# Performance work log

Measured on AMD Instinct MI355X. Metric: run time of the kernel, lower is better.

Reference implementation:

```python
import jax, jax.numpy as jnp
import numpy as np

N_NODES = 50000
N_EDGES = 1600000
IN_DIM, HID_DIM, OUT_DIM = 512, 128, 16


def spmm(edge_src, edge_dst, edge_vals, x):
    # sparse.mm(A, x): out[dst] += A[dst, src] * x[src]
    msgs = edge_vals[:, None] * x[edge_src]  # [E, D]
    return jax.ops.segment_sum(msgs, edge_dst, num_segments=N_NODES)


def setup_inputs() -> dict:
    key = jax.random.key(0)
    k1, k2, k3, k4, k5, k6 = jax.random.split(key, 6)
    feature = jax.random.normal(k1, (N_NODES, IN_DIM), dtype=jnp.float32)
    edge_src = jax.random.randint(k2, (N_EDGES,), 0, N_NODES, dtype=jnp.int32)
    edge_dst = jax.random.randint(k3, (N_EDGES,), 0, N_NODES, dtype=jnp.int32)
    edge_vals = jax.random.uniform(k4, (N_EDGES,), dtype=jnp.float32)
    # kaiming_uniform-style init: bound = sqrt(6 / fan_in) (a=sqrt(5) omitted for simplicity of scale)
    b1 = float(np.sqrt(6.0 / IN_DIM))
    b2 = float(np.sqrt(6.0 / HID_DIM))
    W1 = jax.random.uniform(k5, (IN_DIM, HID_DIM), dtype=jnp.float32, minval=-b1, maxval=b1)
    W2 = jax.random.uniform(k6, (HID_DIM, OUT_DIM), dtype=jnp.float32, minval=-b2, maxval=b2)
    return {"feature": feature, "edge_src": edge_src, "edge_dst": edge_dst,
            "edge_vals": edge_vals, "W1": W1, "W2": W2}


def reference(feature, edge_src, edge_dst, edge_vals, W1, W2):
    # layer 1: dense matmul -> sparse aggregation -> ReLU
    h = jax.nn.relu(spmm(edge_src, edge_dst, edge_vals, feature @ W1))
    # layer 2
    out = spmm(edge_src, edge_dst, edge_vals, h @ W2)
    return out
```

## Files before the change

### kernel.cpp

```cpp
#include <hip/hip_runtime.h>

#define N_NODES 50000
#define N_EDGES 1600000
#define IN_DIM 512
#define HID_DIM 128
#define OUT_DIM 16

#define BKT_SHIFT 6
#define BKT_NODES 64
#define NB ((N_NODES + BKT_NODES - 1) / BKT_NODES)
#define SC_BLOCKS ((N_EDGES + 4095) / 4096)
#define PREP_BLOCKS ((IN_DIM * HID_DIM + 1023) / 1024)
#define NS_CAP 2560

typedef __attribute__((ext_vector_type(8))) __bf16 bf16x8;
typedef __attribute__((ext_vector_type(4))) __bf16 bf16x4;
typedef __attribute__((ext_vector_type(8))) unsigned short ushort8;
typedef __attribute__((ext_vector_type(4))) float f32x4;
typedef __attribute__((ext_vector_type(2))) float f32x2;

static __device__ __forceinline__ unsigned short f2bf(float x) {
    unsigned int u = __float_as_uint(x);
    u += 0x7FFFu + ((u >> 16) & 1u);
    return (unsigned short)(u >> 16);
}
static __device__ __forceinline__ float bf2f(unsigned short v) {
    return __uint_as_float(((unsigned int)v) << 16);
}
static __device__ __forceinline__ unsigned char f2fp8(float x) {
    int pk = __builtin_amdgcn_cvt_pk_fp8_f32(x, x, 0, false);
    return (unsigned char)(pk & 0xFF);
}

__device__ inline int wave_incl_scan(int v) {
    #pragma unroll
    for (int off = 1; off < 64; off <<= 1) {
        int x = __shfl_up(v, off, 64);
        if ((threadIdx.x & 63) >= off) v += x;
    }
    return v;
}


__global__ void zero_bcnt_kernel(int* __restrict__ bcnt) {
    int t = threadIdx.x;
    if (t < NB) bcnt[t] = 0;
}

__global__ __launch_bounds__(1024) void hist_prep_kernel(const int* __restrict__ dst,
                                                         int* __restrict__ bcnt,
                                                         int* __restrict__ blk_hist_T,
                                                         const float* __restrict__ W1,
                                                         unsigned short* __restrict__ Wt) {
    if (blockIdx.x >= SC_BLOCKS) {
        int i = (blockIdx.x - SC_BLOCKS) * 1024 + threadIdx.x;
        if (i < IN_DIM * HID_DIM) {
            int k = i >> 7, col = i & 127;
            Wt[(size_t)col * IN_DIM + k] = f2bf(W1[i]);
        }
        return;
    }
    __shared__ int lc[NB];
    const int t = threadIdx.x;
    for (int b = t; b < NB; b += 1024) lc[b] = 0;
    __syncthreads();
    const int eb = blockIdx.x * 4096 + t * 4;
    if (eb + 4 <= N_EDGES) {
        int4 d4 = *(const int4*)&dst[eb];
        atomicAdd(&lc[d4.x >> BKT_SHIFT], 1);
        atomicAdd(&lc[d4.y >> BKT_SHIFT], 1);
        atomicAdd(&lc[d4.z >> BKT_SHIFT], 1);
        atomicAdd(&lc[d4.w >> BKT_SHIFT], 1);
    } else {
        for (int k = 0; k < 4; k++) {
            int e = eb + k;
            if (e < N_EDGES) atomicAdd(&lc[dst[e] >> BKT_SHIFT], 1);
        }
    }
    __syncthreads();
    for (int b = t; b < NB; b += 1024) {
        int c = lc[b];
        blk_hist_T[(size_t)b * SC_BLOCKS + blockIdx.x] = c;
        if (c) atomicAdd(&bcnt[b], c);
    }
}

__global__ __launch_bounds__(1024) void bucket_scan_kernel(const int* __restrict__ bcnt,
                                                           int* __restrict__ bucket_ptr) {
    __shared__ int wsums[16];
    const int t = threadIdx.x;
    const int lane = t & 63, wid = t >> 6;
    int v = (t < NB) ? bcnt[t] : 0;
    int incl = wave_incl_scan(v);
    if (lane == 63) wsums[wid] = incl;
    __syncthreads();
    if (wid == 0) {
        int wv = (lane < 16) ? wsums[lane] : 0;
        int ws = wave_incl_scan(wv);
        if (lane < 16) wsums[lane] = ws;
    }
    __syncthreads();
    int woff = wid ? wsums[wid - 1] : 0;
    int excl = woff + incl - v;
    if (t < NB) bucket_ptr[t] = excl;
    if (t == NB - 1) bucket_ptr[NB] = excl + v;
}

__global__ __launch_bounds__(512) void base_scan_kernel(const int* __restrict__ bucket_ptr,
                                                        int* __restrict__ blk_hist_T) {
    const int lane = threadIdx.x & 63;
    const int b = blockIdx.x * 8 + (threadIdx.x >> 6);
    if (b >= NB) return;
    int* row = blk_hist_T + (size_t)b * SC_BLOCKS;
    int carry = bucket_ptr[b];
    for (int c0 = 0; c0 < SC_BLOCKS; c0 += 64) {
        int idx = c0 + lane;
        int v = (idx < SC_BLOCKS) ? row[idx] : 0;
        int incl = wave_incl_scan(v);
        if (idx < SC_BLOCKS) row[idx] = carry + incl - v;
        carry += __shfl(incl, 63, 64);
    }
}

__global__ __launch_bounds__(1024) void bucket_scatter_kernel(const int* __restrict__ src,
                                                              const int* __restrict__ dst,
                                                              const float* __restrict__ val,
                                                              const int* __restrict__ blk_hist_T,
                                                              int2* __restrict__ pairs_bkt) {
    __shared__ int cbase[NB];
    const int t = threadIdx.x;
    for (int b = t; b < NB; b += 1024)
        cbase[b] = blk_hist_T[(size_t)b * SC_BLOCKS + blockIdx.x];
    __syncthreads();
    const int eb = blockIdx.x * 4096 + t * 4;
    if (eb + 4 <= N_EDGES) {
        int4 s4 = *(const int4*)&src[eb];
        int4 d4 = *(const int4*)&dst[eb];
        float4 v4 = *(const float4*)&val[eb];
        #pragma unroll
        for (int k = 0; k < 4; k++) {
            int ss = (k == 0) ? s4.x : (k == 1) ? s4.y : (k == 2) ? s4.z : s4.w;
            int dd = (k == 0) ? d4.x : (k == 1) ? d4.y : (k == 2) ? d4.z : d4.w;
            float vv = (k == 0) ? v4.x : (k == 1) ? v4.y : (k == 2) ? v4.z : v4.w;
            int b = dd >> BKT_SHIFT, dl = dd & (BKT_NODES - 1);
            int pos = atomicAdd(&cbase[b], 1);
            int2 pr;
            pr.x = ss | (dl << 16);
            pr.y = __float_as_int(vv);
            pairs_bkt[pos] = pr;
        }
    } else {
        for (int k = 0; k < 4; k++) {
            int e = eb + k;
            if (e < N_EDGES) {
                int dd = dst[e];
                int b = dd >> BKT_SHIFT, dl = dd & (BKT_NODES - 1);
                int pos = atomicAdd(&cbase[b], 1);
                int2 pr;
                pr.x = src[e] | (dl << 16);
                pr.y = __float_as_int(val[e]);
                pairs_bkt[pos] = pr;
            }
        }
    }
}

__global__ __launch_bounds__(512) void node_sort_fused_kernel(const int2* __restrict__ pairs_bkt,
                                                              const int* __restrict__ bucket_ptr,
                                                              int* __restrict__ row_ptr,
                                                              int2* __restrict__ pairs) {
    __shared__ int cnt[BKT_NODES];
    __shared__ int base[BKT_NODES];
    __shared__ int2 stage[NS_CAP];
    const int t = threadIdx.x;
    const int b = blockIdx.x;
    const int s = bucket_ptr[b], e = bucket_ptr[b + 1];
    if (t < BKT_NODES) cnt[t] = 0;
    __syncthreads();
    for (int i = s + t; i < e; i += 512)
        atomicAdd(&cnt[pairs_bkt[i].x >> 16], 1);
    __syncthreads();
    if (t < BKT_NODES) {
        int v = cnt[t];
        int incl = wave_incl_scan(v);
        base[t] = s + incl - v;
    }
    __syncthreads();
    if (t < BKT_NODES) {
        int n = b * BKT_NODES + t;
        if (n < N_NODES) row_ptr[n] = base[t];
        cnt[t] = 0;
    }
    if (b == NB - 1 && t == 0) row_ptr[N_NODES] = N_EDGES;
    __syncthreads();
    for (int i = s + t; i < e; i += 512) {
        int2 pr = pairs_bkt[i];
        int dl = pr.x >> 16;
        int p = base[dl] + atomicAdd(&cnt[dl], 1);
        int loc = p - s;
        if (loc < NS_CAP) stage[loc] = pr;
        else pairs[p] = pr;
    }
    __syncthreads();
    const int lim = min(e - s, NS_CAP);
    for (int j = t; j < lim; j += 512)
        pairs[s + j] = stage[j];
}


#define G1_XSTR 72
#define G1_BSTR 72
__global__ __launch_bounds__(512) void gemm1_kernel(const float* __restrict__ X,
                                                    const unsigned short* __restrict__ Wt,
                                                    unsigned char* __restrict__ h0) {
    __shared__ __align__(16) unsigned short Xs[128 * G1_XSTR];
    __shared__ __align__(16) unsigned short Bs[128 * G1_BSTR];
    const int t = threadIdx.x;
    const int lane = t & 63;
    const int wave = t >> 6;
    const int wr = wave >> 2;
    const int wc = wave & 3;
    const int c = lane & 15, g = lane >> 4;
    const int m0 = blockIdx.x * 128;

    f32x4 acc[4][2];
    #pragma unroll
    for (int mt = 0; mt < 4; mt++)
        #pragma unroll
        for (int nt = 0; nt < 2; nt++) acc[mt][nt] = (f32x4){0.f, 0.f, 0.f, 0.f};

    float4 xr[4];
    ushort8 br[2];

    #define G1_LOAD(kt)                                                                  \
        _Pragma("unroll")                                                                \
        for (int p = 0; p < 4; p++) {                                                    \
            int idx = p * 512 + t;                                                       \
            int xrow = idx >> 4, xseg = idx & 15;                                        \
            int grow = m0 + xrow; grow = (grow < N_NODES) ? grow : (N_NODES - 1);        \
            xr[p] = *(const float4*)&X[(size_t)grow * IN_DIM + (kt) * 64 + xseg * 4];    \
        }                                                                                \
        _Pragma("unroll")                                                                \
        for (int p = 0; p < 2; p++) {                                                    \
            int idx = p * 512 + t;                                                       \
            int bcol = idx >> 3, bseg = idx & 7;                                         \
            br[p] = *(const ushort8*)&Wt[(size_t)bcol * IN_DIM + (kt) * 64 + bseg * 8];  \
        }

    G1_LOAD(0)
    for (int kt = 0; kt < 8; kt++) {
        #pragma unroll
        for (int p = 0; p < 4; p++) {
            int idx = p * 512 + t;
            int xrow = idx >> 4, xseg = idx & 15;
            bf16x4 xw;
            xw[0] = (__bf16)xr[p].x; xw[1] = (__bf16)xr[p].y;
            xw[2] = (__bf16)xr[p].z; xw[3] = (__bf16)xr[p].w;
            *(bf16x4*)&Xs[xrow * G1_XSTR + xseg * 4] = xw;
        }
        #pragma unroll
        for (int p = 0; p < 2; p++) {
            int idx = p * 512 + t;
            int bcol = idx >> 3, bseg = idx & 7;
            *(ushort8*)&Bs[bcol * G1_BSTR + bseg * 8] = br[p];
        }
        __syncthreads();
        if (kt < 7) G1_LOAD(kt + 1)
        #pragma unroll
        for (int ks = 0; ks < 2; ks++) {
            bf16x8 bf[2];
            #pragma unroll
            for (int nt = 0; nt < 2; nt++) {
                int col = wc * 32 + nt * 16 + c;
                bf[nt] = *(const bf16x8*)&Bs[col * G1_BSTR + ks * 32 + g * 8];
            }
            #pragma unroll
            for (int mt = 0; mt < 4; mt++) {
                bf16x8 af = *(const bf16x8*)&Xs[(wr * 64 + mt * 16 + c) * G1_XSTR + ks * 32 + g * 8];
                #pragma unroll
                for (int nt = 0; nt < 2; nt++)
                    acc[mt][nt] = __builtin_amdgcn_mfma_f32_16x16x32_bf16(af, bf[nt],
                                                                          acc[mt][nt], 0, 0, 0);
            }
        }
        __syncthreads();
    }
    #undef G1_LOAD

    #pragma unroll
    for (int mt = 0; mt < 4; mt++) {
        #pragma unroll
        for (int r = 0; r < 4; r++) {
            int row = m0 + wr * 64 + mt * 16 + g * 4 + r;
            if (row < N_NODES) {
                #pragma unroll
                for (int nt = 0; nt < 2; nt++) {
                    int col = wc * 32 + nt * 16 + c;
                    h0[(size_t)row * HID_DIM + col] = f2fp8(acc[mt][nt][r]);
                }
            }
        }
    }
}

__global__ __launch_bounds__(256) void spmm1_node_kernel(const unsigned char* __restrict__ h0,
                                                         const int* __restrict__ row_ptr,
                                                         const int2* __restrict__ pairs,
                                                         unsigned short* __restrict__ h) {
    const int wid = __builtin_amdgcn_readfirstlane(threadIdx.x >> 6);
    const int n = blockIdx.x * 4 + wid;
    const int lane = threadIdx.x & 63;
    const int s = row_ptr[n], e = row_ptr[n + 1];
    const unsigned char* h0l = h0 + lane * 2;
    float ax = 0.f, ay = 0.f;
    for (int base = s; base < e; base += 8) {
        float vv[8];
        const unsigned char* rp[8];
        #pragma unroll
        for (int k = 0; k < 8; k++) {
            int idx = base + k;
            int cidx = (idx < e) ? idx : (e - 1);
            int2 pr = pairs[cidx];
            vv[k] = (idx < e) ? __int_as_float(pr.y) : 0.f;
            rp[k] = h0l + (size_t)(pr.x & 0xFFFF) * HID_DIM;
        }
        unsigned short gg[8];
        #pragma unroll
        for (int k = 0; k < 8; k++) gg[k] = *(const unsigned short*)rp[k];
        #pragma unroll
        for (int k = 0; k < 8; k++) {
            f32x2 f = __builtin_amdgcn_cvt_pk_f32_fp8((int)gg[k], false);
            ax += vv[k] * f.x;
            ay += vv[k] * f.y;
        }
    }
    unsigned int w = ((unsigned int)f2bf(fmaxf(ay, 0.f)) << 16) | f2bf(fmaxf(ax, 0.f));
    ((unsigned int*)(h + (size_t)n * HID_DIM))[lane] = w;
}

__global__ __launch_bounds__(256) void gemm2_kernel(const unsigned short* __restrict__ H,
                                                    const float* __restrict__ W2,
                                                    unsigned short* __restrict__ C) {
    __shared__ float Hs[16][132];
    __shared__ float Ws[128][16];
    const int t = threadIdx.x;
    const int n0 = blockIdx.x * 16;
    #pragma unroll
    for (int p = 0; p < 2; p++) {
        int idx = p * 256 + t;
        ((float4*)Ws)[idx] = ((const float4*)W2)[idx];
    }
    {
        int row = t >> 4, seg = t & 15;
        int gr = n0 + row;
        ushort8 hv = {0, 0, 0, 0, 0, 0, 0, 0};
        if (gr < N_NODES) hv = *(const ushort8*)&H[(size_t)gr * HID_DIM + seg * 8];
        #pragma unroll
        for (int j = 0; j < 8; j++) Hs[row][seg * 8 + j] = bf2f(hv[j]);
    }
    __syncthreads();
    const int nl = t >> 4, j = t & 15;
    float acc = 0.f;
    #pragma unroll 8
    for (int k = 0; k < 128; k++) acc += Hs[nl][k] * Ws[k][j];
    int n = n0 + nl;
    if (n < N_NODES) C[(size_t)n * OUT_DIM + j] = f2bf(acc);
}

__global__ __launch_bounds__(256) void spmm2_node_kernel(const unsigned short* __restrict__ h2,
                                                         const int* __restrict__ row_ptr,
                                                         const int2* __restrict__ pairs,
                                                         float* __restrict__ out) {
    const int idx = blockIdx.x * 256 + threadIdx.x;
    const int n = idx >> 4;
    const int d = idx & 15;
    if (n >= N_NODES) return;
    const int s = row_ptr[n], e = row_ptr[n + 1];
    float acc = 0.f;
    int i = s;
    for (; i + 4 <= e; i += 4) {
        int2 p0 = pairs[i], p1 = pairs[i + 1], p2 = pairs[i + 2], p3 = pairs[i + 3];
        unsigned short g0 = h2[(size_t)(p0.x & 0xFFFF) * OUT_DIM + d];
        unsigned short g1 = h2[(size_t)(p1.x & 0xFFFF) * OUT_DIM + d];
        unsigned short g2 = h2[(size_t)(p2.x & 0xFFFF) * OUT_DIM + d];
        unsigned short g3 = h2[(size_t)(p3.x & 0xFFFF) * OUT_DIM + d];
        acc += __int_as_float(p0.y) * bf2f(g0) + __int_as_float(p1.y) * bf2f(g1)
             + __int_as_float(p2.y) * bf2f(g2) + __int_as_float(p3.y) * bf2f(g3);
    }
    for (; i < e; i++) {
        int2 pr = pairs[i];
        acc += __int_as_float(pr.y) * bf2f(h2[(size_t)(pr.x & 0xFFFF) * OUT_DIM + d]);
    }
    out[(size_t)n * OUT_DIM + d] = acc;
}


extern "C" void kernel_launch(void* const* d_in, const int* in_sizes, int n_in,
                              void* d_out, int out_size, void* d_ws, size_t ws_size,
                              hipStream_t stream) {
    const float* feature   = (const float*)d_in[0];
    const int*   edge_src  = (const int*)d_in[1];
    const int*   edge_dst  = (const int*)d_in[2];
    const float* edge_vals = (const float*)d_in[3];
    const float* W1        = (const float*)d_in[4];
    const float* W2        = (const float*)d_in[5];
    float* out = (float*)d_out;

    char* ws = (char*)d_ws;
    size_t off = 0;
    auto alloc = [&](size_t bytes) {
        void* p = ws + off;
        off += (bytes + 255) & ~(size_t)255;
        return p;
    };
    unsigned char*  h0    = (unsigned char*)alloc((size_t)N_NODES * HID_DIM);
    unsigned short* Wt    = (unsigned short*)alloc((size_t)IN_DIM * HID_DIM * 2);
    unsigned short* h     = (unsigned short*)alloc((size_t)N_NODES * HID_DIM * 2);
    unsigned short* h2    = (unsigned short*)alloc((size_t)N_NODES * OUT_DIM * 2);
    int*   bcnt           = (int*)alloc((size_t)NB * 4);
    int*   bucket_ptr     = (int*)alloc((size_t)(NB + 1) * 4);
    int*   blk_hist_T     = (int*)alloc((size_t)NB * SC_BLOCKS * 4);
    int*   row_ptr        = (int*)alloc((size_t)(N_NODES + 1) * 4);
    int2*  pairs_bkt      = (int2*)alloc((size_t)N_EDGES * 8);
    int2*  pairs          = (int2*)alloc((size_t)N_EDGES * 8);

    zero_bcnt_kernel<<<1, 1024, 0, stream>>>(bcnt);
    hist_prep_kernel<<<SC_BLOCKS + PREP_BLOCKS, 1024, 0, stream>>>(edge_dst, bcnt, blk_hist_T,
                                                                   W1, Wt);
    bucket_scan_kernel<<<1, 1024, 0, stream>>>(bcnt, bucket_ptr);
    base_scan_kernel<<<(NB + 7) / 8, 512, 0, stream>>>(bucket_ptr, blk_hist_T);
    bucket_scatter_kernel<<<SC_BLOCKS, 1024, 0, stream>>>(edge_src, edge_dst, edge_vals,
                                                          blk_hist_T, pairs_bkt);
    node_sort_fused_kernel<<<NB, 512, 0, stream>>>(pairs_bkt, bucket_ptr, row_ptr, pairs);

    gemm1_kernel<<<(N_NODES + 127) / 128, 512, 0, stream>>>(feature, Wt, h0);
    spmm1_node_kernel<<<(N_NODES + 3) / 4, 256, 0, stream>>>(h0, row_ptr, pairs, h);
    gemm2_kernel<<<(N_NODES + 15) / 16, 256, 0, stream>>>(h, W2, h2);
    spmm2_node_kernel<<<(N_NODES * 16 + 255) / 256, 256, 0, stream>>>(h2, row_ptr, pairs, out);
}
```

Measured before the change: 146.5 us.

## Merge bucket scatter with gemm1 launch and fuse gemm2 into spmm1 epilogue

Measured after the change: 168.6 us. 15.1% more time.

```diff
diff --git a/kernel.cpp b/kernel.cpp
--- a/kernel.cpp
+++ b/kernel.cpp
@@ -12,6 +12,7 @@
 #define SC_BLOCKS ((N_EDGES + 4095) / 4096)
 #define PREP_BLOCKS ((IN_DIM * HID_DIM + 1023) / 1024)
 #define NS_CAP 2560
+#define MG_GEMM_BLOCKS ((N_NODES + 127) / 128)
 
 typedef __attribute__((ext_vector_type(8))) __bf16 bf16x8;
 typedef __attribute__((ext_vector_type(4))) __bf16 bf16x4;
@@ -122,44 +123,146 @@
     }
 }
 
-__global__ __launch_bounds__(1024) void bucket_scatter_kernel(const int* __restrict__ src,
-                                                              const int* __restrict__ dst,
-                                                              const float* __restrict__ val,
-                                                              const int* __restrict__ blk_hist_T,
-                                                              int2* __restrict__ pairs_bkt) {
-    __shared__ int cbase[NB];
-    const int t = threadIdx.x;
-    for (int b = t; b < NB; b += 1024)
-        cbase[b] = blk_hist_T[(size_t)b * SC_BLOCKS + blockIdx.x];
-    __syncthreads();
-    const int eb = blockIdx.x * 4096 + t * 4;
-    if (eb + 4 <= N_EDGES) {
-        int4 s4 = *(const int4*)&src[eb];
-        int4 d4 = *(const int4*)&dst[eb];
-        float4 v4 = *(const float4*)&val[eb];
-        #pragma unroll
-        for (int k = 0; k < 4; k++) {
-            int ss = (k == 0) ? s4.x : (k == 1) ? s4.y : (k == 2) ? s4.z : s4.w;
-            int dd = (k == 0) ? d4.x : (k == 1) ? d4.y : (k == 2) ? d4.z : d4.w;
-            float vv = (k == 0) ? v4.x : (k == 1) ? v4.y : (k == 2) ? v4.z : v4.w;
-            int b = dd >> BKT_SHIFT, dl = dd & (BKT_NODES - 1);
-            int pos = atomicAdd(&cbase[b], 1);
-            int2 pr;
-            pr.x = ss | (dl << 16);
-            pr.y = __float_as_int(vv);
-            pairs_bkt[pos] = pr;
+
+#define G1_XSTR 72
+#define G1_BSTR 72
+__global__ __launch_bounds__(512) void scatter_gemm1_kernel(const float* __restrict__ X,
+                                                            const unsigned short* __restrict__ Wt,
+                                                            unsigned char* __restrict__ h0,
+                                                            const int* __restrict__ src,
+                                                            const int* __restrict__ dst,
+                                                            const float* __restrict__ val,
+                                                            const int* __restrict__ blk_hist_T,
+                                                            int2* __restrict__ pairs_bkt) {
+    if (blockIdx.x < MG_GEMM_BLOCKS) {
+        __shared__ __align__(16) unsigned short Xs[128 * G1_XSTR];
+        __shared__ __align__(16) unsigned short Bs[128 * G1_BSTR];
+        const int t = threadIdx.x;
+        const int lane = t & 63;
+        const int wave = t >> 6;
+        const int wr = wave >> 2;
+        const int wc = wave & 3;
+        const int c = lane & 15, g = lane >> 4;
+        const int m0 = blockIdx.x * 128;
+
+        f32x4 acc[4][2];
+        #pragma unroll
+        for (int mt = 0; mt < 4; mt++)
+            #pragma unroll
+            for (int nt = 0; nt < 2; nt++) acc[mt][nt] = (f32x4){0.f, 0.f, 0.f, 0.f};
+
+        float4 xr[4];
+        ushort8 br[2];
+
+        #define G1_LOAD(kt)                                                                  \
+            _Pragma("unroll")                                                                \
+            for (int p = 0; p < 4; p++) {                                                    \
+                int idx = p * 512 + t;                                                       \
+                int xrow = idx >> 4, xseg = idx & 15;                                        \
+                int grow = m0 + xrow; grow = (grow < N_NODES) ? grow : (N_NODES - 1);        \
+                xr[p] = *(const float4*)&X[(size_t)grow * IN_DIM + (kt) * 64 + xseg * 4];    \
+            }                                                                                \
+            _Pragma("unroll")                                                                \
+            for (int p = 0; p < 2; p++) {                                                    \
+                int idx = p * 512 + t;                                                       \
+                int bcol = idx >> 3, bseg = idx & 7;                                         \
+                br[p] = *(const ushort8*)&Wt[(size_t)bcol * IN_DIM + (kt) * 64 + bseg * 8];  \
+            }
+
+        G1_LOAD(0)
+        for (int kt = 0; kt < 8; kt++) {
+            #pragma unroll
+            for (int p = 0; p < 4; p++) {
+                int idx = p * 512 + t;
+                int xrow = idx >> 4, xseg = idx & 15;
+                bf16x4 xw;
+                xw[0] = (__bf16)xr[p].x; xw[1] = (__bf16)xr[p].y;
+                xw[2] = (__bf16)xr[p].z; xw[3] = (__bf16)xr[p].w;
+                *(bf16x4*)&Xs[xrow * G1_XSTR + xseg * 4] = xw;
+            }
+            #pragma unroll
+            for (int p = 0; p < 2; p++) {
+                int idx = p * 512 + t;
+                int bcol = idx >> 3, bseg = idx & 7;
+                *(ushort8*)&Bs[bcol * G1_BSTR + bseg * 8] = br[p];
+            }
+            __syncthreads();
+            if (kt < 7) G1_LOAD(kt + 1)
+            #pragma unroll
+            for (int ks = 0; ks < 2; ks++) {
+                bf16x8 bf[2];
+                #pragma unroll
+                for (int nt = 0; nt < 2; nt++) {
+                    int col = wc * 32 + nt * 16 + c;
+                    bf[nt] = *(const bf16x8*)&Bs[col * G1_BSTR + ks * 32 + g * 8];
+                }
+                #pragma unroll
+                for (int mt = 0; mt < 4; mt++) {
+                    bf16x8 af = *(const bf16x8*)&Xs[(wr * 64 + mt * 16 + c) * G1_XSTR + ks * 32 + g * 8];
+                    #pragma unroll
+                    for (int nt = 0; nt < 2; nt++)
+                        acc[mt][nt] = __builtin_amdgcn_mfma_f32_16x16x32_bf16(af, bf[nt],
+                                                                              acc[mt][nt], 0, 0, 0);
+                }
+            }
+            __syncthreads();
+        }
+        #undef G1_LOAD
+
+        #pragma unroll
+        for (int mt = 0; mt < 4; mt++) {
+            #pragma unroll
+            for (int r = 0; r < 4; r++) {
+                int row = m0 + wr * 64 + mt * 16 + g * 4 + r;
+                if (row < N_NODES) {
+                    #pragma unroll
+                    for (int nt = 0; nt < 2; nt++) {
+                        int col = wc * 32 + nt * 16 + c;
+                        h0[(size_t)row * HID_DIM + col] = f2fp8(acc[mt][nt][r]);
+                    }
+                }
+            }
         }
     } else {
-        for (int k = 0; k < 4; k++) {
-            int e = eb + k;
-            if (e < N_EDGES) {
-                int dd = dst[e];
-                int b = dd >> BKT_SHIFT, dl = dd & (BKT_NODES - 1);
-                int pos = atomicAdd(&cbase[b], 1);
-                int2 pr;
-                pr.x = src[e] | (dl << 16);
-                pr.y = __float_as_int(val[e]);
-                pairs_bkt[pos] = pr;
+        __shared__ int cbase[NB];
+        const int sb = blockIdx.x - MG_GEMM_BLOCKS;
+        const int t = threadIdx.x;
+        for (int b = t; b < NB; b += 512)
+            cbase[b] = blk_hist_T[(size_t)b * SC_BLOCKS + sb];
+        __syncthreads();
+        const int eb = sb * 4096 + t * 8;
+        #pragma unroll
+        for (int half = 0; half < 2; half++) {
+            int e0 = eb + half * 4;
+            if (e0 + 4 <= N_EDGES) {
+                int4 s4 = *(const int4*)&src[e0];
+                int4 d4 = *(const int4*)&dst[e0];
+                float4 v4 = *(const float4*)&val[e0];
+                #pragma unroll
+                for (int k = 0; k < 4; k++) {
+                    int ss = (k == 0) ? s4.x : (k == 1) ? s4.y : (k == 2) ? s4.z : s4.w;
+                    int dd = (k == 0) ? d4.x : (k == 1) ? d4.y : (k == 2) ? d4.z : d4.w;
+                    float vv = (k == 0) ? v4.x : (k == 1) ? v4.y : (k == 2) ? v4.z : v4.w;
+                    int b = dd >> BKT_SHIFT, dl = dd & (BKT_NODES - 1);
+                    int pos = atomicAdd(&cbase[b], 1);
+                    int2 pr;
+                    pr.x = ss | (dl << 16);
+                    pr.y = __float_as_int(vv);
+                    pairs_bkt[pos] = pr;
+                }
+            } else {
+                for (int k = 0; k < 4; k++) {
+                    int e = e0 + k;
+                    if (e < N_EDGES) {
+                        int dd = dst[e];
+                        int b = dd >> BKT_SHIFT, dl = dd & (BKT_NODES - 1);
+                        int pos = atomicAdd(&cbase[b], 1);
+                        int2 pr;
+                        pr.x = src[e] | (dl << 16);
+                        pr.y = __float_as_int(val[e]);
+                        pairs_bkt[pos] = pr;
+                    }
+                }
             }
         }
     }
@@ -207,106 +310,20 @@
         pairs[s + j] = stage[j];
 }
 
-
-#define G1_XSTR 72
-#define G1_BSTR 72
-__global__ __launch_bounds__(512) void gemm1_kernel(const float* __restrict__ X,
-                                                    const unsigned short* __restrict__ Wt,
-                                                    unsigned char* __restrict__ h0) {
-    __shared__ __align__(16) unsigned short Xs[128 * G1_XSTR];
-    __shared__ __align__(16) unsigned short Bs[128 * G1_BSTR];
+__global__ __launch_bounds__(256) void spmm1_fused_kernel(const unsigned char* __restrict__ h0,
+                                                          const int* __restrict__ row_ptr,
+                                                          const int2* __restrict__ pairs,
+                                                          const float* __restrict__ W2,
+                                                          unsigned short* __restrict__ h2) {
+    __shared__ float W2s[HID_DIM][OUT_DIM + 1];
     const int t = threadIdx.x;
-    const int lane = t & 63;
-    const int wave = t >> 6;
-    const int wr = wave >> 2;
-    const int wc = wave & 3;
-    const int c = lane & 15, g = lane >> 4;
-    const int m0 = blockIdx.x * 128;
-
-    f32x4 acc[4][2];
     #pragma unroll
-    for (int mt = 0; mt < 4; mt++)
-        #pragma unroll
-        for (int nt = 0; nt < 2; nt++) acc[mt][nt] = (f32x4){0.f, 0.f, 0.f, 0.f};
-
-    float4 xr[4];
-    ushort8 br[2];
-
-    #define G1_LOAD(kt)                                                                  \
-        _Pragma("unroll")                                                                \
-        for (int p = 0; p < 4; p++) {                                                    \
-            int idx = p * 512 + t;                                                       \
-            int xrow = idx >> 4, xseg = idx & 15;                                        \
-            int grow = m0 + xrow; grow = (grow < N_NODES) ? grow : (N_NODES - 1);        \
-            xr[p] = *(const float4*)&X[(size_t)grow * IN_DIM + (kt) * 64 + xseg * 4];    \
-        }                                                                                \
-        _Pragma("unroll")                                                                \
-        for (int p = 0; p < 2; p++) {                                                    \
-            int idx = p * 512 + t;                                                       \
-            int bcol = idx >> 3, bseg = idx & 7;                                         \
-            br[p] = *(const ushort8*)&Wt[(size_t)bcol * IN_DIM + (kt) * 64 + bseg * 8];  \
-        }
-
-    G1_LOAD(0)
-    for (int kt = 0; kt < 8; kt++) {
-        #pragma unroll
-        for (int p = 0; p < 4; p++) {
-            int idx = p * 512 + t;
-            int xrow = idx >> 4, xseg = idx & 15;
-            bf16x4 xw;
-            xw[0] = (__bf16)xr[p].x; xw[1] = (__bf16)xr[p].y;
-            xw[2] = (__bf16)xr[p].z; xw[3] = (__bf16)xr[p].w;
-            *(bf16x4*)&Xs[xrow * G1_XSTR + xseg * 4] = xw;
-        }
-        #pragma unroll
-        for (int p = 0; p < 2; p++) {
-            int idx = p * 512 + t;
-            int bcol = idx >> 3, bseg = idx & 7;
-            *(ushort8*)&Bs[bcol * G1_BSTR + bseg * 8] = br[p];
-        }
-        __syncthreads();
-        if (kt < 7) G1_LOAD(kt + 1)
-        #pragma unroll
-        for (int ks = 0; ks < 2; ks++) {
-            bf16x8 bf[2];
-            #pragma unroll
-            for (int nt = 0; nt < 2; nt++) {
-                int col = wc * 32 + nt * 16 + c;
-                bf[nt] = *(const bf16x8*)&Bs[col * G1_BSTR + ks * 32 + g * 8];
-            }
-            #pragma unroll
-            for (int mt = 0; mt < 4; mt++) {
-                bf16x8 af = *(const bf16x8*)&Xs[(wr * 64 + mt * 16 + c) * G1_XSTR + ks * 32 + g * 8];
-                #pragma unroll
-                for (int nt = 0; nt < 2; nt++)
-                    acc[mt][nt] = __builtin_amdgcn_mfma_f32_16x16x32_bf16(af, bf[nt],
-                                                                          acc[mt][nt], 0, 0, 0);
-            }
-        }
-        __syncthreads();
-    }
-    #undef G1_LOAD
-
-    #pragma unroll
-    for (int mt = 0; mt < 4; mt++) {
-        #pragma unroll
-        for (int r = 0; r < 4; r++) {
-            int row = m0 + wr * 64 + mt * 16 + g * 4 + r;
-            if (row < N_NODES) {
-                #pragma unroll
-                for (int nt = 0; nt < 2; nt++) {
-                    int col = wc * 32 + nt * 16 + c;
-                    h0[(size_t)row * HID_DIM + col] = f2fp8(acc[mt][nt][r]);
-                }
-            }
-        }
-    }
-}
-
-__global__ __launch_bounds__(256) void spmm1_node_kernel(const unsigned char* __restrict__ h0,
-                                                         const int* __restrict__ row_ptr,
-                                                         const int2* __restrict__ pairs,
-                                                         unsigned short* __restrict__ h) {
+    for (int p = 0; p < 8; p++) {
+        int idx = p * 256 + t;
+        W2s[idx >> 4][idx & 15] = W2[idx];
+    }
+    __syncthreads();
+
     const int wid = __builtin_amdgcn_readfirstlane(threadIdx.x >> 6);
     const int n = blockIdx.x * 4 + wid;
     const int lane = threadIdx.x & 63;
@@ -334,37 +351,26 @@
             ay += vv[k] * f.y;
         }
     }
-    unsigned int w = ((unsigned int)f2bf(fmaxf(ay, 0.f)) << 16) | f2bf(fmaxf(ax, 0.f));
-    ((unsigned int*)(h + (size_t)n * HID_DIM))[lane] = w;
-}
-
-__global__ __launch_bounds__(256) void gemm2_kernel(const unsigned short* __restrict__ H,
-                                                    const float* __restrict__ W2,
-                                                    unsigned short* __restrict__ C) {
-    __shared__ float Hs[16][132];
-    __shared__ float Ws[128][16];
-    const int t = threadIdx.x;
-    const int n0 = blockIdx.x * 16;
+    const float hx = fmaxf(ax, 0.f), hy = fmaxf(ay, 0.f);
+
+    float p[OUT_DIM];
     #pragma unroll
-    for (int p = 0; p < 2; p++) {
-        int idx = p * 256 + t;
-        ((float4*)Ws)[idx] = ((const float4*)W2)[idx];
-    }
-    {
-        int row = t >> 4, seg = t & 15;
-        int gr = n0 + row;
-        ushort8 hv = {0, 0, 0, 0, 0, 0, 0, 0};
-        if (gr < N_NODES) hv = *(const ushort8*)&H[(size_t)gr * HID_DIM + seg * 8];
-        #pragma unroll
-        for (int j = 0; j < 8; j++) Hs[row][seg * 8 + j] = bf2f(hv[j]);
-    }
-    __syncthreads();
-    const int nl = t >> 4, j = t & 15;
-    float acc = 0.f;
-    #pragma unroll 8
-    for (int k = 0; k < 128; k++) acc += Hs[nl][k] * Ws[k][j];
-    int n = n0 + nl;
-    if (n < N_NODES) C[(size_t)n * OUT_DIM + j] = f2bf(acc);
+    for (int j = 0; j < OUT_DIM; j++)
+        p[j] = hx * W2s[2 * lane][j] + hy * W2s[2 * lane + 1][j];
+    #pragma unroll
+    for (int m = 1; m < 64; m <<= 1)
+        #pragma unroll
+        for (int j = 0; j < OUT_DIM; j++)
+            p[j] += __shfl_xor(p[j], m, 64);
+
+    if (lane == 0) {
+        ushort8 o0, o1;
+        #pragma unroll
+        for (int j = 0; j < 8; j++) { o0[j] = f2bf(p[j]); o1[j] = f2bf(p[8 + j]); }
+        ushort8* dstp = (ushort8*)&h2[(size_t)n * OUT_DIM];
+        dstp[0] = o0;
+        dstp[1] = o1;
+    }
 }
 
 __global__ __launch_bounds__(256) void spmm2_node_kernel(const unsigned short* __restrict__ h2,
@@ -415,7 +421,6 @@
     };
     unsigned char*  h0    = (unsigned char*)alloc((size_t)N_NODES * HID_DIM);
     unsigned short* Wt    = (unsigned short*)alloc((size_t)IN_DIM * HID_DIM * 2);
-    unsigned short* h     = (unsigned short*)alloc((size_t)N_NODES * HID_DIM * 2);
     unsigned short* h2    = (unsigned short*)alloc((size_t)N_NODES * OUT_DIM * 2);
     int*   bcnt           = (int*)alloc((size_t)NB * 4);
     int*   bucket_ptr     = (int*)alloc((size_t)(NB + 1) * 4);
@@ -429,12 +434,10 @@
                                                                    W1, Wt);
     bucket_scan_kernel<<<1, 1024, 0, stream>>>(bcnt, bucket_ptr);
     base_scan_kernel<<<(NB + 7) / 8, 512, 0, stream>>>(bucket_ptr, blk_hist_T);
-    bucket_scatter_kernel<<<SC_BLOCKS, 1024, 0, stream>>>(edge_src, edge_dst, edge_vals,
-                                                          blk_hist_T, pairs_bkt);
+    scatter_gemm1_kernel<<<MG_GEMM_BLOCKS + SC_BLOCKS, 512, 0, stream>>>(
+        feature, Wt, h0, edge_src, edge_dst, edge_vals, blk_hist_T, pairs_bkt);
     node_sort_fused_kernel<<<NB, 512, 0, stream>>>(pairs_bkt, bucket_ptr, row_ptr, pairs);
 
-    gemm1_kernel<<<(N_NODES + 127) / 128, 512, 0, stream>>>(feature, Wt, h0);
-    spmm1_node_kernel<<<(N_NODES + 3) / 4, 256, 0, stream>>>(h0, row_ptr, pairs, h);
-    gemm2_kernel<<<(N_NODES + 15) / 16, 256, 0, stream>>>(h, W2, h2);
+    spmm1_fused_kernel<<<(N_NODES + 3) / 4, 256, 0, stream>>>(h0, row_ptr, pairs, W2, h2);
     spmm2_node_kernel<<<(N_NODES * 16 + 255) / 256, 256, 0, stream>>>(h2, row_ptr, pairs, out);
 }
```

## Merge bucket scatter into gemm1 launch as heterogeneous blocks

Applied to the files above, without the earlier changes.

After: 143.9 us. No clear change (-1.8%).

```diff
diff --git a/kernel.cpp b/kernel.cpp
--- a/kernel.cpp
+++ b/kernel.cpp
@@ -12,6 +12,7 @@
 #define SC_BLOCKS ((N_EDGES + 4095) / 4096)
 #define PREP_BLOCKS ((IN_DIM * HID_DIM + 1023) / 1024)
 #define NS_CAP 2560
+#define MG_GEMM_BLOCKS ((N_NODES + 127) / 128)
 
 typedef __attribute__((ext_vector_type(8))) __bf16 bf16x8;
 typedef __attribute__((ext_vector_type(4))) __bf16 bf16x4;
@@ -122,44 +123,146 @@
     }
 }
 
-__global__ __launch_bounds__(1024) void bucket_scatter_kernel(const int* __restrict__ src,
-                                                              const int* __restrict__ dst,
-                                                              const float* __restrict__ val,
-                                                              const int* __restrict__ blk_hist_T,
-                                                              int2* __restrict__ pairs_bkt) {
-    __shared__ int cbase[NB];
-    const int t = threadIdx.x;
-    for (int b = t; b < NB; b += 1024)
-        cbase[b] = blk_hist_T[(size_t)b * SC_BLOCKS + blockIdx.x];
-    __syncthreads();
-    const int eb = blockIdx.x * 4096 + t * 4;
-    if (eb + 4 <= N_EDGES) {
-        int4 s4 = *(const int4*)&src[eb];
-        int4 d4 = *(const int4*)&dst[eb];
-        float4 v4 = *(const float4*)&val[eb];
-        #pragma unroll
-        for (int k = 0; k < 4; k++) {
-            int ss = (k == 0) ? s4.x : (k == 1) ? s4.y : (k == 2) ? s4.z : s4.w;
-            int dd = (k == 0) ? d4.x : (k == 1) ? d4.y : (k == 2) ? d4.z : d4.w;
-            float vv = (k == 0) ? v4.x : (k == 1) ? v4.y : (k == 2) ? v4.z : v4.w;
-            int b = dd >> BKT_SHIFT, dl = dd & (BKT_NODES - 1);
-            int pos = atomicAdd(&cbase[b], 1);
-            int2 pr;
-            pr.x = ss | (dl << 16);
-            pr.y = __float_as_int(vv);
-            pairs_bkt[pos] = pr;
+
+#define G1_XSTR 72
+#define G1_BSTR 72
+__global__ __launch_bounds__(512) void scatter_gemm1_kernel(const float* __restrict__ X,
+                                                            const unsigned short* __restrict__ Wt,
+                                                            unsigned char* __restrict__ h0,
+                                                            const int* __restrict__ src,
+                                                            const int* __restrict__ dst,
+                                                            const float* __restrict__ val,
+                                                            const int* __restrict__ blk_hist_T,
+                                                            int2* __restrict__ pairs_bkt) {
+    if (blockIdx.x < MG_GEMM_BLOCKS) {
+        __shared__ __align__(16) unsigned short Xs[128 * G1_XSTR];
+        __shared__ __align__(16) unsigned short Bs[128 * G1_BSTR];
+        const int t = threadIdx.x;
+        const int lane = t & 63;
+        const int wave = t >> 6;
+        const int wr = wave >> 2;
+        const int wc = wave & 3;
+        const int c = lane & 15, g = lane >> 4;
+        const int m0 = blockIdx.x * 128;
+
+        f32x4 acc[4][2];
+        #pragma unroll
+        for (int mt = 0; mt < 4; mt++)
+            #pragma unroll
+            for (int nt = 0; nt < 2; nt++) acc[mt][nt] = (f32x4){0.f, 0.f, 0.f, 0.f};
+
+        float4 xr[4];
+        ushort8 br[2];
+
+        #define G1_LOAD(kt)                                                                  \
+            _Pragma("unroll")                                                                \
+            for (int p = 0; p < 4; p++) {                                                    \
+                int idx = p * 512 + t;                                                       \
+                int xrow = idx >> 4, xseg = idx & 15;                                        \
+                int grow = m0 + xrow; grow = (grow < N_NODES) ? grow : (N_NODES - 1);        \
+                xr[p] = *(const float4*)&X[(size_t)grow * IN_DIM + (kt) * 64 + xseg * 4];    \
+            }                                                                                \
+            _Pragma("unroll")                                                                \
+            for (int p = 0; p < 2; p++) {                                                    \
+                int idx = p * 512 + t;                                                       \
+                int bcol = idx >> 3, bseg = idx & 7;                                         \
+                br[p] = *(const ushort8*)&Wt[(size_t)bcol * IN_DIM + (kt) * 64 + bseg * 8];  \
+            }
+
+        G1_LOAD(0)
+        for (int kt = 0; kt < 8; kt++) {
+            #pragma unroll
+            for (int p = 0; p < 4; p++) {
+                int idx = p * 512 + t;
+                int xrow = idx >> 4, xseg = idx & 15;
+                bf16x4 xw;
+                xw[0] = (__bf16)xr[p].x; xw[1] = (__bf16)xr[p].y;
+                xw[2] = (__bf16)xr[p].z; xw[3] = (__bf16)xr[p].w;
+                *(bf16x4*)&Xs[xrow * G1_XSTR + xseg * 4] = xw;
+            }
+            #pragma unroll
+            for (int p = 0; p < 2; p++) {
+                int idx = p * 512 + t;
+                int bcol = idx >> 3, bseg = idx & 7;
+                *(ushort8*)&Bs[bcol * G1_BSTR + bseg * 8] = br[p];
+            }
+            __syncthreads();
+            if (kt < 7) G1_LOAD(kt + 1)
+            #pragma unroll
+            for (int ks = 0; ks < 2; ks++) {
+                bf16x8 bf[2];
+                #pragma unroll
+                for (int nt = 0; nt < 2; nt++) {
+                    int col = wc * 32 + nt * 16 + c;
+                    bf[nt] = *(const bf16x8*)&Bs[col * G1_BSTR + ks * 32 + g * 8];
+                }
+                #pragma unroll
+                for (int mt = 0; mt < 4; mt++) {
+                    bf16x8 af = *(const bf16x8*)&Xs[(wr * 64 + mt * 16 + c) * G1_XSTR + ks * 32 + g * 8];
+                    #pragma unroll
+                    for (int nt = 0; nt < 2; nt++)
+                        acc[mt][nt] = __builtin_amdgcn_mfma_f32_16x16x32_bf16(af, bf[nt],
+                                                                              acc[mt][nt], 0, 0, 0);
+                }
+            }
+            __syncthreads();
+        }
+        #undef G1_LOAD
+
+        #pragma unroll
+        for (int mt = 0; mt < 4; mt++) {
+            #pragma unroll
+            for (int r = 0; r < 4; r++) {
+                int row = m0 + wr * 64 + mt * 16 + g * 4 + r;
+                if (row < N_NODES) {
+                    #pragma unroll
+                    for (int nt = 0; nt < 2; nt++) {
+                        int col = wc * 32 + nt * 16 + c;
+                        h0[(size_t)row * HID_DIM + col] = f2fp8(acc[mt][nt][r]);
+                    }
+                }
+            }
         }
     } else {
-        for (int k = 0; k < 4; k++) {
-            int e = eb + k;
-            if (e < N_EDGES) {
-                int dd = dst[e];
-                int b = dd >> BKT_SHIFT, dl = dd & (BKT_NODES - 1);
-                int pos = atomicAdd(&cbase[b], 1);
-                int2 pr;
-                pr.x = src[e] | (dl << 16);
-                pr.y = __float_as_int(val[e]);
-                pairs_bkt[pos] = pr;
+        __shared__ int cbase[NB];
+        const int sb = blockIdx.x - MG_GEMM_BLOCKS;
+        const int t = threadIdx.x;
+        for (int b = t; b < NB; b += 512)
+            cbase[b] = blk_hist_T[(size_t)b * SC_BLOCKS + sb];
+        __syncthreads();
+        const int eb = sb * 4096 + t * 8;
+        #pragma unroll
+        for (int half = 0; half < 2; half++) {
+            int e0 = eb + half * 4;
+            if (e0 + 4 <= N_EDGES) {
+                int4 s4 = *(const int4*)&src[e0];
+                int4 d4 = *(const int4*)&dst[e0];
+                float4 v4 = *(const float4*)&val[e0];
+                #pragma unroll
+                for (int k = 0; k < 4; k++) {
+                    int ss = (k == 0) ? s4.x : (k == 1) ? s4.y : (k == 2) ? s4.z : s4.w;
+                    int dd = (k == 0) ? d4.x : (k == 1) ? d4.y : (k == 2) ? d4.z : d4.w;
+                    float vv = (k == 0) ? v4.x : (k == 1) ? v4.y : (k == 2) ? v4.z : v4.w;
+                    int b = dd >> BKT_SHIFT, dl = dd & (BKT_NODES - 1);
+                    int pos = atomicAdd(&cbase[b], 1);
+                    int2 pr;
+                    pr.x = ss | (dl << 16);
+                    pr.y = __float_as_int(vv);
+                    pairs_bkt[pos] = pr;
+                }
+            } else {
+                for (int k = 0; k < 4; k++) {
+                    int e = e0 + k;
+                    if (e < N_EDGES) {
+                        int dd = dst[e];
+                        int b = dd >> BKT_SHIFT, dl = dd & (BKT_NODES - 1);
+                        int pos = atomicAdd(&cbase[b], 1);
+                        int2 pr;
+                        pr.x = src[e] | (dl << 16);
+                        pr.y = __float_as_int(val[e]);
+                        pairs_bkt[pos] = pr;
+                    }
+                }
             }
         }
     }
@@ -207,101 +310,6 @@
         pairs[s + j] = stage[j];
 }
 
-
-#define G1_XSTR 72
-#define G1_BSTR 72
-__global__ __launch_bounds__(512) void gemm1_kernel(const float* __restrict__ X,
-                                                    const unsigned short* __restrict__ Wt,
-                                                    unsigned char* __restrict__ h0) {
-    __shared__ __align__(16) unsigned short Xs[128 * G1_XSTR];
-    __shared__ __align__(16) unsigned short Bs[128 * G1_BSTR];
-    const int t = threadIdx.x;
-    const int lane = t & 63;
-    const int wave = t >> 6;
-    const int wr = wave >> 2;
-    const int wc = wave & 3;
-    const int c = lane & 15, g = lane >> 4;
-    const int m0 = blockIdx.x * 128;
-
-    f32x4 acc[4][2];
-    #pragma unroll
-    for (int mt = 0; mt < 4; mt++)
-        #pragma unroll
-        for (int nt = 0; nt < 2; nt++) acc[mt][nt] = (f32x4){0.f, 0.f, 0.f, 0.f};
-
-    float4 xr[4];
-    ushort8 br[2];
-
-    #define G1_LOAD(kt)                                                                  \
-        _Pragma("unroll")                                                                \
-        for (int p = 0; p < 4; p++) {                                                    \
-            int idx = p * 512 + t;                                                       \
-            int xrow = idx >> 4, xseg = idx & 15;                                        \
-            int grow = m0 + xrow; grow = (grow < N_NODES) ? grow : (N_NODES - 1);        \
-            xr[p] = *(const float4*)&X[(size_t)grow * IN_DIM + (kt) * 64 + xseg * 4];    \
-        }                                                                                \
-        _Pragma("unroll")                                                                \
-        for (int p = 0; p < 2; p++) {                                                    \
-            int idx = p * 512 + t;                                                       \
-            int bcol = idx >> 3, bseg = idx & 7;                                         \
-            br[p] = *(const ushort8*)&Wt[(size_t)bcol * IN_DIM + (kt) * 64 + bseg * 8];  \
-        }
-
-    G1_LOAD(0)
-    for (int kt = 0; kt < 8; kt++) {
-        #pragma unroll
-        for (int p = 0; p < 4; p++) {
-            int idx = p * 512 + t;
-            int xrow = idx >> 4, xseg = idx & 15;
-            bf16x4 xw;
-            xw[0] = (__bf16)xr[p].x; xw[1] = (__bf16)xr[p].y;
-            xw[2] = (__bf16)xr[p].z; xw[3] = (__bf16)xr[p].w;
-            *(bf16x4*)&Xs[xrow * G1_XSTR + xseg * 4] = xw;
-        }
-        #pragma unroll
-        for (int p = 0; p < 2; p++) {
-            int idx = p * 512 + t;
-            int bcol = idx >> 3, bseg = idx & 7;
-            *(ushort8*)&Bs[bcol * G1_BSTR + bseg * 8] = br[p];
-        }
-        __syncthreads();
-        if (kt < 7) G1_LOAD(kt + 1)
-        #pragma unroll
-        for (int ks = 0; ks < 2; ks++) {
-            bf16x8 bf[2];
-            #pragma unroll
-            for (int nt = 0; nt < 2; nt++) {
-                int col = wc * 32 + nt * 16 + c;
-                bf[nt] = *(const bf16x8*)&Bs[col * G1_BSTR + ks * 32 + g * 8];
-            }
-            #pragma unroll
-            for (int mt = 0; mt < 4; mt++) {
-                bf16x8 af = *(const bf16x8*)&Xs[(wr * 64 + mt * 16 + c) * G1_XSTR + ks * 32 + g * 8];
-                #pragma unroll
-                for (int nt = 0; nt < 2; nt++)
-                    acc[mt][nt] = __builtin_amdgcn_mfma_f32_16x16x32_bf16(af, bf[nt],
-                                                                          acc[mt][nt], 0, 0, 0);
-            }
-        }
-        __syncthreads();
-    }
-    #undef G1_LOAD
-
-    #pragma unroll
-    for (int mt = 0; mt < 4; mt++) {
-        #pragma unroll
-        for (int r = 0; r < 4; r++) {
-            int row = m0 + wr * 64 + mt * 16 + g * 4 + r;
-            if (row < N_NODES) {
-                #pragma unroll
-                for (int nt = 0; nt < 2; nt++) {
-                    int col = wc * 32 + nt * 16 + c;
-                    h0[(size_t)row * HID_DIM + col] = f2fp8(acc[mt][nt][r]);
-                }
-            }
-        }
-    }
-}
 
 __global__ __launch_bounds__(256) void spmm1_node_kernel(const unsigned char* __restrict__ h0,
                                                          const int* __restrict__ row_ptr,
@@ -429,11 +437,10 @@
                                                                    W1, Wt);
     bucket_scan_kernel<<<1, 1024, 0, stream>>>(bcnt, bucket_ptr);
     base_scan_kernel<<<(NB + 7) / 8, 512, 0, stream>>>(bucket_ptr, blk_hist_T);
-    bucket_scatter_kernel<<<SC_BLOCKS, 1024, 0, stream>>>(edge_src, edge_dst, edge_vals,
-                                                          blk_hist_T, pairs_bkt);
+    scatter_gemm1_kernel<<<MG_GEMM_BLOCKS + SC_BLOCKS, 512, 0, stream>>>(
+        feature, Wt, h0, edge_src, edge_dst, edge_vals, blk_hist_T, pairs_bkt);
     node_sort_fused_kernel<<<NB, 512, 0, stream>>>(pairs_bkt, bucket_ptr, row_ptr, pairs);
 
-    gemm1_kernel<<<(N_NODES + 127) / 128, 512, 0, stream>>>(feature, Wt, h0);
     spmm1_node_kernel<<<(N_NODES + 3) / 4, 256, 0, stream>>>(h0, row_ptr, pairs, h);
     gemm2_kernel<<<(N_NODES + 15) / 16, 256, 0, stream>>>(h, W2, h2);
     spmm2_node_kernel<<<(N_NODES * 16 + 255) / 256, 256, 0, stream>>>(h2, row_ptr, pairs, out);
```
